# Performance work log

Hardware: AMD Instinct MI355X
Metric: run time of the kernel (lower is better)

The kernel has to match this reference:

```python
import jax, jax.numpy as jnp
import numpy as np

SCALE = 0.1  # ContraNorm scale hyperparameter (init arg)
EPS = 1e-12  # torch F.normalize default eps

def setup_inputs() -> dict:
    key = jax.random.key(0)
    N, D = 16384, 256
    x = jax.random.normal(key, (N, D), dtype=jnp.float32)
    return {"x": x}

def reference(x):
    # L2-normalize each row (torch F.normalize with dim=1)
    norm = jnp.linalg.norm(x, axis=1, keepdims=True)
    x_norm = x / jnp.maximum(norm, EPS)
    # cosine similarity [N, N], row-softmax
    sim = jax.nn.softmax(x_norm @ x_norm.T, axis=1)
    # residual blend: (1+s) x - s * sim @ x
    return (1.0 + SCALE) * x - SCALE * (sim @ x)
```

## Files before the change

### kernel.cpp

```cpp
#include <hip/hip_runtime.h>
#include <stdint.h>


typedef __bf16 bf16x8 __attribute__((ext_vector_type(8)));
typedef float f32x16 __attribute__((ext_vector_type(16)));
typedef unsigned short u16;
typedef unsigned int u32;

#define GLBP __attribute__((address_space(1)))
#define LDSP __attribute__((address_space(3)))

#define NROW 16384
#define DIMD 256

__device__ __forceinline__ void g2l16(const void* g, void* l) {
  __builtin_amdgcn_global_load_lds((const GLBP u32*)g, (LDSP u32*)l, 16, 0, 0);
}

__device__ __forceinline__ u32 cvt_pk(float lo, float hi) {
  u32 r;
  asm("v_cvt_pk_bf16_f32 %0, %1, %2" : "=v"(r) : "v"(lo), "v"(hi));
  return r;
}

__device__ __forceinline__ u16 f2b(float f) {
  union { __bf16 h; u16 u; } cv; cv.h = (__bf16)f; return cv.u;
}

__global__ void cn_norm(const float* __restrict__ x, unsigned char* __restrict__ xn) {
  const int w = threadIdx.x >> 6, l = threadIdx.x & 63;
  const int row = blockIdx.x * 4 + w;
  const float4 v = *(const float4*)(x + row * DIMD + l * 4);
  float s = v.x * v.x + v.y * v.y + v.z * v.z + v.w * v.w;
#pragma unroll
  for (int m = 1; m < 64; m <<= 1) s += __shfl_xor(s, m, 64);
  const float inv = 1.0f / fmaxf(sqrtf(s), 1e-12f);
  ushort4 o;
  o.x = f2b(v.x * inv); o.y = f2b(v.y * inv);
  o.z = f2b(v.z * inv); o.w = f2b(v.w * inv);
  const int lf = (((l >> 1) & 1) << 5) + (row & 31);
  *(ushort4*)(xn + (row >> 5) * 16384 + (l >> 2) * 1024 + lf * 16 + ((l & 1) << 3)) = o;
}

__global__ void cn_vtpack(const float* __restrict__ x, unsigned char* __restrict__ vt) {
  __shared__ u16 Lx[32][264];
  const int t = threadIdx.x, kb = blockIdx.x;
  {
    const int row = t >> 3, d0 = (t & 7) * 32;
    const float* src = x + (size_t)(kb * 32 + row) * DIMD + d0;
#pragma unroll
    for (int i = 0; i < 8; ++i) {
      const float4 v = *(const float4*)(src + i * 4);
      Lx[row][d0 + i * 4 + 0] = f2b(v.x);
      Lx[row][d0 + i * 4 + 1] = f2b(v.y);
      Lx[row][d0 + i * 4 + 2] = f2b(v.z);
      Lx[row][d0 + i * 4 + 3] = f2b(v.w);
    }
  }
  __syncthreads();
#pragma unroll
  for (int gi = 0; gi < 4; ++gi) {
    const int G = gi * 256 + t;
    const int fr = G >> 6, ln = G & 63;
    const int d = (fr >> 1) * 32 + (ln & 31);
    const int k0 = (fr & 1) * 16 + (ln >> 5) * 8;
    u16 pk[8];
#pragma unroll
    for (int j = 0; j < 8; ++j) pk[j] = Lx[k0 + j][d];
    *(uint4*)(vt + kb * 16384 + fr * 1024 + ln * 16) = *(const uint4*)pk;
  }
}

template <int NS, bool DIRECT>
__global__ __launch_bounds__(256, 2) void cn_flash(
    const unsigned char* __restrict__ xn,
    const unsigned char* __restrict__ vt,
    unsigned char* __restrict__ Po,
    float* __restrict__ Ls,
    const float* __restrict__ x,
    float* __restrict__ out) {
  constexpr int SH = (NS == 4) ? 2 : (NS == 2) ? 1 : 0;
  constexpr int KT = NROW / (32 * NS);
  __shared__ __align__(16) unsigned char sK[2][16384];
  __shared__ __align__(16) unsigned char sV[2][16384];
  const int tid = threadIdx.x;
  const int w = tid >> 6, l = tid & 63;
  const int bid = blockIdx.x;
  const int split = bid & (NS - 1), qblk = bid >> SH;
  const int q0 = qblk * 128 + w * 32;
  const int lq = l & 31, hi = l >> 5;

  const size_t gbase = (size_t)split * KT * 16384;
#pragma unroll
  for (int r = 0; r < 4; ++r) {
    g2l16(xn + gbase + r * 4096 + tid * 16, &sK[0][r * 4096 + tid * 16]);
    g2l16(vt + gbase + r * 4096 + tid * 16, &sV[0][r * 4096 + tid * 16]);
  }
  bf16x8 Qf[16];
  {
    const unsigned char* qb = xn + (size_t)(q0 >> 5) * 16384;
#pragma unroll
    for (int f = 0; f < 16; ++f) Qf[f] = *(const bf16x8*)(qb + f * 1024 + l * 16);
  }

  f32x16 O[8];
#pragma unroll
  for (int c = 0; c < 8; ++c)
#pragma unroll
    for (int r = 0; r < 16; ++r) O[c][r] = 0.f;
  float lsum = 0.f;

  __syncthreads();

  for (int t = 0; t < KT; ++t) {
    const int cur = t & 1;
    if (t + 1 < KT) {
      const size_t gt = gbase + (size_t)(t + 1) * 16384;
      const int nb = cur ^ 1;
#pragma unroll
      for (int r = 0; r < 4; ++r) {
        g2l16(xn + gt + r * 4096 + tid * 16, &sK[nb][r * 4096 + tid * 16]);
        g2l16(vt + gt + r * 4096 + tid * 16, &sV[nb][r * 4096 + tid * 16]);
      }
    }
    const unsigned char* Kb = &sK[cur][0];
    const unsigned char* Vb = &sV[cur][0];

    f32x16 St;
#pragma unroll
    for (int r = 0; r < 16; ++r) St[r] = 0.f;
#pragma unroll
    for (int f = 0; f < 16; ++f) {
      const bf16x8 ka = *(const bf16x8*)(Kb + f * 1024 + l * 16);
      St = __builtin_amdgcn_mfma_f32_32x32x16_bf16(ka, Qf[f], St, 0, 0, 0);
    }

    float p[16];
#pragma unroll
    for (int r = 0; r < 16; ++r) {
      p[r] = __expf(St[r] - 1.0f);
      lsum += p[r];
    }
    u32 a0 = cvt_pk(p[0], p[1]), a1 = cvt_pk(p[2], p[3]);
    u32 b0 = cvt_pk(p[4], p[5]), b1 = cvt_pk(p[6], p[7]);
    asm("v_permlane32_swap_b32 %0, %1" : "+v"(a0), "+v"(b0));
    asm("v_permlane32_swap_b32 %0, %1" : "+v"(a1), "+v"(b1));
    u32 c0 = cvt_pk(p[8], p[9]), c1 = cvt_pk(p[10], p[11]);
    u32 d0 = cvt_pk(p[12], p[13]), d1 = cvt_pk(p[14], p[15]);
    asm("v_permlane32_swap_b32 %0, %1" : "+v"(c0), "+v"(d0));
    asm("v_permlane32_swap_b32 %0, %1" : "+v"(c1), "+v"(d1));
    union PW { u32 w[4]; bf16x8 v; } pf0, pf1;
    pf0.w[0] = a0; pf0.w[1] = a1; pf0.w[2] = b0; pf0.w[3] = b1;
    pf1.w[0] = c0; pf1.w[1] = c1; pf1.w[2] = d0; pf1.w[3] = d1;

#pragma unroll
    for (int c = 0; c < 8; ++c) {
      const bf16x8 va0 = *(const bf16x8*)(Vb + (c * 2 + 0) * 1024 + l * 16);
      O[c] = __builtin_amdgcn_mfma_f32_32x32x16_bf16(va0, pf0.v, O[c], 0, 0, 0);
      const bf16x8 va1 = *(const bf16x8*)(Vb + (c * 2 + 1) * 1024 + l * 16);
      O[c] = __builtin_amdgcn_mfma_f32_32x32x16_bf16(va1, pf1.v, O[c], 0, 0, 0);
    }
    __syncthreads();
  }

  const int qc = q0 + lq;
  if (DIRECT) {
    const float Lt = lsum + __shfl_xor(lsum, 32, 64);
    const float sc = 0.1f / Lt;
#pragma unroll
    for (int c = 0; c < 8; ++c)
#pragma unroll
      for (int r = 0; r < 16; ++r) {
        const int d = c * 32 + (r & 3) + 8 * (r >> 2) + 4 * hi;
        out[(size_t)qc * DIMD + d] =
            1.1f * x[(size_t)qc * DIMD + d] - sc * O[c][r];
      }
  } else {
#pragma unroll
    for (int c = 0; c < 8; ++c)
#pragma unroll
      for (int r = 0; r < 16; ++r) {
        const int d = c * 32 + (r & 3) + 8 * (r >> 2) + 4 * hi;
        *(u16*)(Po + ((size_t)split * DIMD + d) * 32768 + (size_t)qc * 2) = f2b(O[c][r]);
      }
    Ls[(size_t)(split * 2 + hi) * NROW + qc] = lsum;
  }
}

template <int NS>
__global__ void cn_merge(const float* __restrict__ x,
                         const unsigned char* __restrict__ Po,
                         const float* __restrict__ Ls,
                         float* __restrict__ out) {
  __shared__ float acc[256][65];
  __shared__ float Lq[64];
  const int t = threadIdx.x;
  const int q0 = blockIdx.x * 64;
  const int dloc = t >> 3, ch = t & 7;
#pragma unroll
  for (int pass = 0; pass < 8; ++pass) {
    const int d = pass * 32 + dloc;
    float a[8] = {0.f, 0.f, 0.f, 0.f, 0.f, 0.f, 0.f, 0.f};
#pragma unroll
    for (int s = 0; s < NS; ++s) {
      const uint4 v = *(const uint4*)(Po + ((size_t)(s * 256 + d)) * 32768 +
                                      (size_t)q0 * 2 + ch * 16);
      const u32 wv[4] = {v.x, v.y, v.z, v.w};
#pragma unroll
      for (int k = 0; k < 4; ++k) {
        a[2 * k + 0] += __uint_as_float(wv[k] << 16);
        a[2 * k + 1] += __uint_as_float(wv[k] & 0xffff0000u);
      }
    }
#pragma unroll
    for (int j = 0; j < 8; ++j) acc[d][ch * 8 + j] = a[j];
  }
  if (t < 64) {
    const int q = q0 + t;
    float L = 0.f;
#pragma unroll
    for (int s = 0; s < NS; ++s)
      L += Ls[(size_t)(s * 2 + 0) * NROW + q] + Ls[(size_t)(s * 2 + 1) * NROW + q];
    Lq[t] = 1.0f / L;
  }
  __syncthreads();
  const int ql = t >> 2, dd0 = (t & 3) * 64;
  const float inv = Lq[ql];
  const int q = q0 + ql;
#pragma unroll
  for (int i = 0; i < 64; i += 4) {
    const float4 xv = *(const float4*)(x + (size_t)q * DIMD + dd0 + i);
    float4 ov;
    ov.x = 1.1f * xv.x - 0.1f * acc[dd0 + i + 0][ql] * inv;
    ov.y = 1.1f * xv.y - 0.1f * acc[dd0 + i + 1][ql] * inv;
    ov.z = 1.1f * xv.z - 0.1f * acc[dd0 + i + 2][ql] * inv;
    ov.w = 1.1f * xv.w - 0.1f * acc[dd0 + i + 3][ql] * inv;
    *(float4*)(out + (size_t)q * DIMD + dd0 + i) = ov;
  }
}

extern "C" void kernel_launch(void* const* d_in, const int* in_sizes, int n_in,
                              void* d_out, int out_size, void* d_ws, size_t ws_size,
                              hipStream_t stream) {
  const float* x = (const float*)d_in[0];
  float* out = (float*)d_out;
  unsigned char* xn = (unsigned char*)d_ws;
  unsigned char* vt = xn + (size_t)8 * 1024 * 1024;
  unsigned char* Po = vt + (size_t)8 * 1024 * 1024;

  cn_norm<<<4096, 256, 0, stream>>>(x, xn);
  cn_vtpack<<<512, 256, 0, stream>>>(x, vt);

  const size_t need4 = (size_t)(16 + 32) * 1024 * 1024 + 512 * 1024;
  const size_t need2 = (size_t)(16 + 16) * 1024 * 1024 + 256 * 1024;
  if (ws_size >= need4) {
    float* Ls = (float*)(Po + (size_t)4 * 8 * 1024 * 1024);
    cn_flash<4, false><<<512, 256, 0, stream>>>(xn, vt, Po, Ls, x, out);
    cn_merge<4><<<256, 256, 0, stream>>>(x, Po, Ls, out);
  } else if (ws_size >= need2) {
    float* Ls = (float*)(Po + (size_t)2 * 8 * 1024 * 1024);
    cn_flash<2, false><<<256, 256, 0, stream>>>(xn, vt, Po, Ls, x, out);
    cn_merge<2><<<256, 256, 0, stream>>>(x, Po, Ls, out);
  } else {
    cn_flash<1, true><<<128, 256, 0, stream>>>(xn, vt, nullptr, nullptr, x, out);
  }
}
```

Measured before the change: 318.0 us.

## Read V mostly from global, enlarge K tiles, add 8-way KV split

Restructures the flash loop so each iteration stages two 32-row K tiles in LDS. Only the last V chunk goes through LDS; the other seven V fragments are read straight from global memory (L2). It adds s_setprio around the MFMA blocks and computes exp via exp2f with a folded log2e scale. It also adds an 8-way key split path with 1024 blocks when workspace allows. The goal is to cut LDS traffic and footprint and raise parallelism, at the risk of global-load latency stalls on the V operands and more merge work.

```diff
diff --git a/kernel.cpp b/kernel.cpp
--- a/kernel.cpp
+++ b/kernel.cpp
@@ -79,10 +79,11 @@
     float* __restrict__ Ls,
     const float* __restrict__ x,
     float* __restrict__ out) {
-  constexpr int SH = (NS == 4) ? 2 : (NS == 2) ? 1 : 0;
-  constexpr int KT = NROW / (32 * NS);
-  __shared__ __align__(16) unsigned char sK[2][16384];
-  __shared__ __align__(16) unsigned char sV[2][16384];
+  constexpr int SH = (NS == 8) ? 3 : (NS == 4) ? 2 : (NS == 2) ? 1 : 0;
+  constexpr int KB32 = NROW / (32 * NS);
+  constexpr int KT2 = KB32 / 2;
+  __shared__ __align__(16) unsigned char sK[2][32768];
+  __shared__ __align__(16) unsigned char sVq[2][4096];
   const int tid = threadIdx.x;
   const int w = tid >> 6, l = tid & 63;
   const int bid = blockIdx.x;
@@ -90,12 +91,15 @@
   const int q0 = qblk * 128 + w * 32;
   const int lq = l & 31, hi = l >> 5;
 
-  const size_t gbase = (size_t)split * KT * 16384;
-#pragma unroll
-  for (int r = 0; r < 4; ++r) {
-    g2l16(xn + gbase + r * 4096 + tid * 16, &sK[0][r * 4096 + tid * 16]);
-    g2l16(vt + gbase + r * 4096 + tid * 16, &sV[0][r * 4096 + tid * 16]);
-  }
+  const size_t gbase = (size_t)split * KB32 * 16384;
+  const int vchunk = tid >> 7, voffb = (tid & 127) * 16;
+#pragma unroll
+  for (int r = 0; r < 8; ++r) {
+    const int off = r * 4096 + tid * 16;
+    g2l16(xn + gbase + off, &sK[0][off]);
+  }
+  g2l16(vt + gbase + (size_t)vchunk * 16384 + 14336 + voffb, &sVq[0][vchunk * 2048 + voffb]);
+
   bf16x8 Qf[16];
   {
     const unsigned char* qb = xn + (size_t)(q0 >> 5) * 16384;
@@ -109,56 +113,73 @@
 #pragma unroll
     for (int r = 0; r < 16; ++r) O[c][r] = 0.f;
   float lsum = 0.f;
+  const float L2E = 1.442695041f;
 
   __syncthreads();
 
-  for (int t = 0; t < KT; ++t) {
-    const int cur = t & 1;
-    if (t + 1 < KT) {
-      const size_t gt = gbase + (size_t)(t + 1) * 16384;
+  for (int T = 0; T < KT2; ++T) {
+    const int cur = T & 1;
+    if (T + 1 < KT2) {
+      const size_t gt = gbase + (size_t)(T + 1) * 32768;
       const int nb = cur ^ 1;
 #pragma unroll
-      for (int r = 0; r < 4; ++r) {
-        g2l16(xn + gt + r * 4096 + tid * 16, &sK[nb][r * 4096 + tid * 16]);
-        g2l16(vt + gt + r * 4096 + tid * 16, &sV[nb][r * 4096 + tid * 16]);
-      }
-    }
-    const unsigned char* Kb = &sK[cur][0];
-    const unsigned char* Vb = &sV[cur][0];
-
-    f32x16 St;
-#pragma unroll
-    for (int r = 0; r < 16; ++r) St[r] = 0.f;
-#pragma unroll
-    for (int f = 0; f < 16; ++f) {
-      const bf16x8 ka = *(const bf16x8*)(Kb + f * 1024 + l * 16);
-      St = __builtin_amdgcn_mfma_f32_32x32x16_bf16(ka, Qf[f], St, 0, 0, 0);
-    }
-
-    float p[16];
-#pragma unroll
-    for (int r = 0; r < 16; ++r) {
-      p[r] = __expf(St[r] - 1.0f);
-      lsum += p[r];
-    }
-    u32 a0 = cvt_pk(p[0], p[1]), a1 = cvt_pk(p[2], p[3]);
-    u32 b0 = cvt_pk(p[4], p[5]), b1 = cvt_pk(p[6], p[7]);
-    asm("v_permlane32_swap_b32 %0, %1" : "+v"(a0), "+v"(b0));
-    asm("v_permlane32_swap_b32 %0, %1" : "+v"(a1), "+v"(b1));
-    u32 c0 = cvt_pk(p[8], p[9]), c1 = cvt_pk(p[10], p[11]);
-    u32 d0 = cvt_pk(p[12], p[13]), d1 = cvt_pk(p[14], p[15]);
-    asm("v_permlane32_swap_b32 %0, %1" : "+v"(c0), "+v"(d0));
-    asm("v_permlane32_swap_b32 %0, %1" : "+v"(c1), "+v"(d1));
-    union PW { u32 w[4]; bf16x8 v; } pf0, pf1;
-    pf0.w[0] = a0; pf0.w[1] = a1; pf0.w[2] = b0; pf0.w[3] = b1;
-    pf1.w[0] = c0; pf1.w[1] = c1; pf1.w[2] = d0; pf1.w[3] = d1;
-
-#pragma unroll
-    for (int c = 0; c < 8; ++c) {
-      const bf16x8 va0 = *(const bf16x8*)(Vb + (c * 2 + 0) * 1024 + l * 16);
-      O[c] = __builtin_amdgcn_mfma_f32_32x32x16_bf16(va0, pf0.v, O[c], 0, 0, 0);
-      const bf16x8 va1 = *(const bf16x8*)(Vb + (c * 2 + 1) * 1024 + l * 16);
-      O[c] = __builtin_amdgcn_mfma_f32_32x32x16_bf16(va1, pf1.v, O[c], 0, 0, 0);
+      for (int r = 0; r < 8; ++r) {
+        const int off = r * 4096 + tid * 16;
+        g2l16(xn + gt + off, &sK[nb][off]);
+      }
+      g2l16(vt + gt + (size_t)vchunk * 16384 + 14336 + voffb,
+            &sVq[nb][vchunk * 2048 + voffb]);
+    }
+#pragma unroll
+    for (int ss = 0; ss < 2; ++ss) {
+      const unsigned char* Kb = &sK[cur][ss * 16384];
+      const bf16x8* Vg = (const bf16x8*)(vt + gbase + ((size_t)(2 * T + ss)) * 16384);
+      const unsigned char* Vq = &sVq[cur][ss * 2048];
+
+      f32x16 St;
+#pragma unroll
+      for (int r = 0; r < 16; ++r) St[r] = 0.f;
+      __builtin_amdgcn_s_setprio(1);
+#pragma unroll
+      for (int f = 0; f < 16; ++f) {
+        const bf16x8 ka = *(const bf16x8*)(Kb + f * 1024 + l * 16);
+        St = __builtin_amdgcn_mfma_f32_32x32x16_bf16(ka, Qf[f], St, 0, 0, 0);
+      }
+      __builtin_amdgcn_s_setprio(0);
+
+      float p[16];
+#pragma unroll
+      for (int r = 0; r < 16; ++r) {
+        p[r] = exp2f(fmaf(St[r], L2E, -L2E));
+        lsum += p[r];
+      }
+      u32 a0 = cvt_pk(p[0], p[1]), a1 = cvt_pk(p[2], p[3]);
+      u32 b0 = cvt_pk(p[4], p[5]), b1 = cvt_pk(p[6], p[7]);
+      asm("v_permlane32_swap_b32 %0, %1" : "+v"(a0), "+v"(b0));
+      asm("v_permlane32_swap_b32 %0, %1" : "+v"(a1), "+v"(b1));
+      u32 c0 = cvt_pk(p[8], p[9]), c1 = cvt_pk(p[10], p[11]);
+      u32 d0 = cvt_pk(p[12], p[13]), d1 = cvt_pk(p[14], p[15]);
+      asm("v_permlane32_swap_b32 %0, %1" : "+v"(c0), "+v"(d0));
+      asm("v_permlane32_swap_b32 %0, %1" : "+v"(c1), "+v"(d1));
+      union PW { u32 w[4]; bf16x8 v; } pf0, pf1;
+      pf0.w[0] = a0; pf0.w[1] = a1; pf0.w[2] = b0; pf0.w[3] = b1;
+      pf1.w[0] = c0; pf1.w[1] = c1; pf1.w[2] = d0; pf1.w[3] = d1;
+
+      __builtin_amdgcn_s_setprio(1);
+#pragma unroll
+      for (int c = 0; c < 7; ++c) {
+        const bf16x8 va0 = Vg[(c * 2 + 0) * 64 + l];
+        O[c] = __builtin_amdgcn_mfma_f32_32x32x16_bf16(va0, pf0.v, O[c], 0, 0, 0);
+        const bf16x8 va1 = Vg[(c * 2 + 1) * 64 + l];
+        O[c] = __builtin_amdgcn_mfma_f32_32x32x16_bf16(va1, pf1.v, O[c], 0, 0, 0);
+      }
+      {
+        const bf16x8 va0 = *(const bf16x8*)(Vq + l * 16);
+        O[7] = __builtin_amdgcn_mfma_f32_32x32x16_bf16(va0, pf0.v, O[7], 0, 0, 0);
+        const bf16x8 va1 = *(const bf16x8*)(Vq + 1024 + l * 16);
+        O[7] = __builtin_amdgcn_mfma_f32_32x32x16_bf16(va1, pf1.v, O[7], 0, 0, 0);
+      }
+      __builtin_amdgcn_s_setprio(0);
     }
     __syncthreads();
   }
@@ -251,9 +272,14 @@
   cn_norm<<<4096, 256, 0, stream>>>(x, xn);
   cn_vtpack<<<512, 256, 0, stream>>>(x, vt);
 
+  const size_t need8 = (size_t)(16 + 64) * 1024 * 1024 + 1024 * 1024;
   const size_t need4 = (size_t)(16 + 32) * 1024 * 1024 + 512 * 1024;
   const size_t need2 = (size_t)(16 + 16) * 1024 * 1024 + 256 * 1024;
-  if (ws_size >= need4) {
+  if (ws_size >= need8) {
+    float* Ls = (float*)(Po + (size_t)8 * 8 * 1024 * 1024);
+    cn_flash<8, false><<<1024, 256, 0, stream>>>(xn, vt, Po, Ls, x, out);
+    cn_merge<8><<<256, 256, 0, stream>>>(x, Po, Ls, out);
+  } else if (ws_size >= need4) {
     float* Ls = (float*)(Po + (size_t)4 * 8 * 1024 * 1024);
     cn_flash<4, false><<<512, 256, 0, stream>>>(xn, vt, Po, Ls, x, out);
     cn_merge<4><<<256, 256, 0, stream>>>(x, Po, Ls, out);
```

New measurement: 478.6 us. 1.5x slower.

## Load first quarter of V tile directly from global, shrink V LDS buffer

Applied to the files above, without the earlier changes.

The first 4 KB of each V tile (output columns 0-63) is now read straight from global/L2 into registers instead of being staged through LDS. This shrinks the V LDS buffer from 16 KB to 12 KB per stage. The aim is to cut LDS footprint and LDS read traffic, and the change also adds s_setprio around the MFMA sections, uses exp2 with an FMA-folded scale, and tree-reduces the row sum. The risk is that the global loads, issued after the QK MFMAs, may not hide their latency before the PV MFMAs need them, and the MFMA order over O is changed.

```diff
diff --git a/kernel.cpp b/kernel.cpp
--- a/kernel.cpp
+++ b/kernel.cpp
@@ -79,10 +79,10 @@
     float* __restrict__ Ls,
     const float* __restrict__ x,
     float* __restrict__ out) {
-  constexpr int SH = (NS == 4) ? 2 : (NS == 2) ? 1 : 0;
+  constexpr int SH = (NS == 8) ? 3 : (NS == 4) ? 2 : (NS == 2) ? 1 : 0;
   constexpr int KT = NROW / (32 * NS);
   __shared__ __align__(16) unsigned char sK[2][16384];
-  __shared__ __align__(16) unsigned char sV[2][16384];
+  __shared__ __align__(16) unsigned char sV[2][12288];
   const int tid = threadIdx.x;
   const int w = tid >> 6, l = tid & 63;
   const int bid = blockIdx.x;
@@ -92,10 +92,12 @@
 
   const size_t gbase = (size_t)split * KT * 16384;
 #pragma unroll
-  for (int r = 0; r < 4; ++r) {
+  for (int r = 0; r < 4; ++r)
     g2l16(xn + gbase + r * 4096 + tid * 16, &sK[0][r * 4096 + tid * 16]);
-    g2l16(vt + gbase + r * 4096 + tid * 16, &sV[0][r * 4096 + tid * 16]);
-  }
+#pragma unroll
+  for (int r = 0; r < 3; ++r)
+    g2l16(vt + gbase + 4096 + r * 4096 + tid * 16, &sV[0][r * 4096 + tid * 16]);
+
   bf16x8 Qf[16];
   {
     const unsigned char* qb = xn + (size_t)(q0 >> 5) * 16384;
@@ -109,6 +111,7 @@
 #pragma unroll
     for (int r = 0; r < 16; ++r) O[c][r] = 0.f;
   float lsum = 0.f;
+  const float L2E = 1.442695041f;
 
   __syncthreads();
 
@@ -118,10 +121,11 @@
       const size_t gt = gbase + (size_t)(t + 1) * 16384;
       const int nb = cur ^ 1;
 #pragma unroll
-      for (int r = 0; r < 4; ++r) {
+      for (int r = 0; r < 4; ++r)
         g2l16(xn + gt + r * 4096 + tid * 16, &sK[nb][r * 4096 + tid * 16]);
-        g2l16(vt + gt + r * 4096 + tid * 16, &sV[nb][r * 4096 + tid * 16]);
-      }
+#pragma unroll
+      for (int r = 0; r < 3; ++r)
+        g2l16(vt + gt + 4096 + r * 4096 + tid * 16, &sV[nb][r * 4096 + tid * 16]);
     }
     const unsigned char* Kb = &sK[cur][0];
     const unsigned char* Vb = &sV[cur][0];
@@ -129,17 +133,29 @@
     f32x16 St;
 #pragma unroll
     for (int r = 0; r < 16; ++r) St[r] = 0.f;
+    __builtin_amdgcn_s_setprio(1);
 #pragma unroll
     for (int f = 0; f < 16; ++f) {
       const bf16x8 ka = *(const bf16x8*)(Kb + f * 1024 + l * 16);
       St = __builtin_amdgcn_mfma_f32_32x32x16_bf16(ka, Qf[f], St, 0, 0, 0);
     }
+    __builtin_amdgcn_s_setprio(0);
+
+    const bf16x8* Vg = (const bf16x8*)(vt + gbase + (size_t)t * 16384);
+    const bf16x8 vg0 = Vg[0 * 64 + l];
+    const bf16x8 vg1 = Vg[1 * 64 + l];
+    const bf16x8 vg2 = Vg[2 * 64 + l];
+    const bf16x8 vg3 = Vg[3 * 64 + l];
 
     float p[16];
 #pragma unroll
-    for (int r = 0; r < 16; ++r) {
-      p[r] = __expf(St[r] - 1.0f);
-      lsum += p[r];
+    for (int r = 0; r < 16; ++r) p[r] = exp2f(fmaf(St[r], L2E, -L2E));
+    {
+      float s0 = (p[0] + p[1]) + (p[2] + p[3]);
+      float s1 = (p[4] + p[5]) + (p[6] + p[7]);
+      float s2 = (p[8] + p[9]) + (p[10] + p[11]);
+      float s3 = (p[12] + p[13]) + (p[14] + p[15]);
+      lsum += (s0 + s1) + (s2 + s3);
     }
     u32 a0 = cvt_pk(p[0], p[1]), a1 = cvt_pk(p[2], p[3]);
     u32 b0 = cvt_pk(p[4], p[5]), b1 = cvt_pk(p[6], p[7]);
@@ -153,13 +169,22 @@
     pf0.w[0] = a0; pf0.w[1] = a1; pf0.w[2] = b0; pf0.w[3] = b1;
     pf1.w[0] = c0; pf1.w[1] = c1; pf1.w[2] = d0; pf1.w[3] = d1;
 
-#pragma unroll
-    for (int c = 0; c < 8; ++c) {
-      const bf16x8 va0 = *(const bf16x8*)(Vb + (c * 2 + 0) * 1024 + l * 16);
-      O[c] = __builtin_amdgcn_mfma_f32_32x32x16_bf16(va0, pf0.v, O[c], 0, 0, 0);
-      const bf16x8 va1 = *(const bf16x8*)(Vb + (c * 2 + 1) * 1024 + l * 16);
-      O[c] = __builtin_amdgcn_mfma_f32_32x32x16_bf16(va1, pf1.v, O[c], 0, 0, 0);
-    }
+    __builtin_amdgcn_s_setprio(1);
+    O[0] = __builtin_amdgcn_mfma_f32_32x32x16_bf16(vg0, pf0.v, O[0], 0, 0, 0);
+    O[1] = __builtin_amdgcn_mfma_f32_32x32x16_bf16(vg2, pf0.v, O[1], 0, 0, 0);
+#pragma unroll
+    for (int c = 2; c < 8; ++c) {
+      const bf16x8 va = *(const bf16x8*)(Vb + (c * 2 - 4) * 1024 + l * 16);
+      O[c] = __builtin_amdgcn_mfma_f32_32x32x16_bf16(va, pf0.v, O[c], 0, 0, 0);
+    }
+    O[0] = __builtin_amdgcn_mfma_f32_32x32x16_bf16(vg1, pf1.v, O[0], 0, 0, 0);
+    O[1] = __builtin_amdgcn_mfma_f32_32x32x16_bf16(vg3, pf1.v, O[1], 0, 0, 0);
+#pragma unroll
+    for (int c = 2; c < 8; ++c) {
+      const bf16x8 va = *(const bf16x8*)(Vb + (c * 2 - 3) * 1024 + l * 16);
+      O[c] = __builtin_amdgcn_mfma_f32_32x32x16_bf16(va, pf1.v, O[c], 0, 0, 0);
+    }
+    __builtin_amdgcn_s_setprio(0);
     __syncthreads();
   }
 
```

Result: slower. 340.5 us (+7.1%).
